# Optimization experiments

Hardware: AMD Instinct MI355X
Metric: run time of the kernel (lower is better)

The kernel has to match this reference:

```python
import jax, jax.numpy as jnp
import numpy as np

SEQ_LENGTH = 256
MID_O = 800
OUT_DIM = 128

def _lstm_cell(x, h, c, Wih, Whh, bih, bhh):
    # PyTorch gate order: i, f, g, o
    gates = x @ Wih.T + h @ Whh.T + bih + bhh
    i, f, g, o = jnp.split(gates, 4, axis=-1)
    c = jax.nn.sigmoid(f) * c + jax.nn.sigmoid(i) * jnp.tanh(g)
    h = jax.nn.sigmoid(o) * jnp.tanh(c)
    return h, c

def _lstm_layer(x_seq, Wih, Whh, bih, bhh):
    B = x_seq.shape[1]
    H = Whh.shape[1]
    h0 = jnp.zeros((B, H), x_seq.dtype)
    c0 = jnp.zeros((B, H), x_seq.dtype)
    def step(carry, xt):
        h, c = carry
        h, c = _lstm_cell(xt, h, c, Wih, Whh, bih, bhh)
        return (h, c), h
    (hT, cT), out = jax.lax.scan(step, (h0, c0), x_seq)
    return out, hT, cT

def _lstm_params(key, in_dim, hid, scale=0.05):
    k1, k2, k3, k4 = jax.random.split(key, 4)
    return (jax.random.normal(k1, (4 * hid, in_dim), jnp.float32) * scale,
            jax.random.normal(k2, (4 * hid, hid), jnp.float32) * scale,
            jax.random.normal(k3, (4 * hid,), jnp.float32) * scale,
            jax.random.normal(k4, (4 * hid,), jnp.float32) * scale)

def setup_inputs() -> dict:
    key = jax.random.key(0)
    ks = jax.random.split(key, 10)
    input_dim, mid_i, latent, mid_o, out_dim = 128, 60, 20, MID_O, OUT_DIM
    x = jax.random.normal(ks[0], (SEQ_LENGTH, 1024, input_dim), jnp.float32)
    fc1 = _lstm_params(ks[1], input_dim, mid_i)
    fc21 = _lstm_params(ks[2], mid_i, latent)
    l3 = _lstm_params(ks[3], latent, latent)
    l4 = _lstm_params(ks[4], latent, mid_o)
    l5 = _lstm_params(ks[5], mid_o, out_dim)
    id_W = jax.random.normal(ks[6], (latent, latent), jnp.float32) * 0.05
    id_b = jnp.zeros((latent,), jnp.float32)
    down_W = jax.random.normal(ks[7], (latent, out_dim), jnp.float32) * 0.05
    down_b = jnp.zeros((latent,), jnp.float32)
    d = {"x": x,
         "fc1_Wih": fc1[0], "fc1_Whh": fc1[1], "fc1_bih": fc1[2], "fc1_bhh": fc1[3],
         "fc21_Wih": fc21[0], "fc21_Whh": fc21[1], "fc21_bih": fc21[2], "fc21_bhh": fc21[3],
         "l3_Wih": l3[0], "l3_Whh": l3[1], "l3_bih": l3[2], "l3_bhh": l3[3],
         "l4_Wih": l4[0], "l4_Whh": l4[1], "l4_bih": l4[2], "l4_bhh": l4[3],
         "l5_Wih": l5[0], "l5_Whh": l5[1], "l5_bih": l5[2], "l5_bhh": l5[3],
         "id_W": id_W, "id_b": id_b, "down_W": down_W, "down_b": down_b}
    return d

def reference(x, fc1_Wih, fc1_Whh, fc1_bih, fc1_bhh,
              fc21_Wih, fc21_Whh, fc21_bih, fc21_bhh,
              l3_Wih, l3_Whh, l3_bih, l3_bhh,
              l4_Wih, l4_Whh, l4_bih, l4_bhh,
              l5_Wih, l5_Whh, l5_bih, l5_bhh,
              id_W, id_b, down_W, down_b):
    # ---- encode ----
    out1, _, _ = _lstm_layer(x, fc1_Wih, fc1_Whh, fc1_bih, fc1_bhh)
    h1 = jax.nn.relu(out1)
    _, mu, c_mean = _lstm_layer(h1, fc21_Wih, fc21_Whh, fc21_bih, fc21_bhh)
    # ---- decode (deterministic: z = mu, c_t = cell_mean) ----
    B = mu.shape[0]
    output0 = mu @ id_W.T + id_b
    h2 = jnp.zeros((B, MID_O), x.dtype); c2 = jnp.zeros((B, MID_O), x.dtype)
    h3 = jnp.zeros((B, OUT_DIM), x.dtype); c3 = jnp.zeros((B, OUT_DIM), x.dtype)
    def step(carry, _):
        h, c, h2, c2, h3, c3, out = carry
        h, c = _lstm_cell(out, h, c, l3_Wih, l3_Whh, l3_bih, l3_bhh)
        h2, c2 = _lstm_cell(h, h2, c2, l4_Wih, l4_Whh, l4_bih, l4_bhh)
        h3, c3 = _lstm_cell(h2, h3, c3, l5_Wih, l5_Whh, l5_bih, l5_bhh)
        out = h3 @ down_W.T + down_b
        return (h, c, h2, c2, h3, c3, out), h3
    _, outMean = jax.lax.scan(step, (mu, c_mean, h2, c2, h3, c3, output0), None, length=SEQ_LENGTH)
    return outMean, mu
```

## Files before the change

### kernel.cpp

```cpp
#include <hip/hip_runtime.h>
#include <stdint.h>

typedef __bf16 bf16x8 __attribute__((ext_vector_type(8)));
typedef float  f32x4  __attribute__((ext_vector_type(4)));

static __device__ __forceinline__ unsigned short f2bf(float f) {
  unsigned int u = __float_as_uint(f);
  u = u + 0x7fffu + ((u >> 16) & 1u);
  return (unsigned short)(u >> 16);
}
static __device__ __forceinline__ float bf2f(unsigned short h) {
  return __uint_as_float(((unsigned int)h) << 16);
}
static __device__ __forceinline__ float sigm(float x) {
  return 1.f / (1.f + __expf(-x));
}
static __device__ __forceinline__ float tanh_f(float x) {
  float ax = fabsf(x);
  float e = __expf(-2.f * ax);
  float t = (1.f - e) / (1.f + e);
  return copysignf(t, x);
}

__global__ void kPrep(const float* __restrict__ w4i, const float* __restrict__ w4h,
                      const float* __restrict__ b4i, const float* __restrict__ b4h,
                      const float* __restrict__ w5i, const float* __restrict__ w5h,
                      const float* __restrict__ b5i, const float* __restrict__ b5h,
                      const float* __restrict__ w1i, const float* __restrict__ w1h,
                      const float* __restrict__ b1i, const float* __restrict__ b1h,
                      const float* __restrict__ w2i, const float* __restrict__ w2h,
                      const float* __restrict__ b2i, const float* __restrict__ b2h,
                      const float* __restrict__ w3i, const float* __restrict__ w3h,
                      const float* __restrict__ b3i, const float* __restrict__ b3h,
                      unsigned short* __restrict__ W4F, unsigned short* __restrict__ W5,
                      float* __restrict__ W1, float* __restrict__ W2, float* __restrict__ W3,
                      float* __restrict__ b4, float* __restrict__ b5,
                      float* __restrict__ b1, float* __restrict__ b2, float* __restrict__ b3) {
  int idx0 = blockIdx.x * blockDim.x + threadIdx.x;
  int stride = gridDim.x * blockDim.x;
  const int TOT = 3197328;
  for (int i = idx0; i < TOT; i += stride) {
    int i2 = i;
    if (i2 < 2662400) {
      int T = i2 / 13312;
      int r1 = i2 % 13312;
      int kc = r1 / 512;
      int e = r1 % 512;
      int lane = e >> 3, j = e & 7;
      int q = lane >> 4, l16 = lane & 15;
      int gate = ((T & 1) ? 2 : 0) + (l16 >> 3);
      int col = (T >> 1) * 8 + (l16 & 7);
      int wrow = gate * 800 + col;
      int k = kc * 32 + q * 8 + j;
      float v = (k < 20) ? w4i[wrow * 20 + k]
                         : ((k >= 24 && k < 824) ? w4h[wrow * 800 + (k - 24)] : 0.f);
      W4F[i2] = f2bf(v);
      continue;
    }
    i2 -= 2662400;
    if (i2 < 475136) {
      int n = i2 / 928, k = i2 % 928;
      float v = (k < 800) ? w5i[n * 800 + k] : w5h[n * 128 + (k - 800)];
      W5[i2] = f2bf(v);
      continue;
    }
    i2 -= 475136;
    if (i2 < 46080) {
      int n = i2 / 192, k = i2 % 192;
      W1[i2] = (k < 128) ? w1i[n * 128 + k] : ((k < 188) ? w1h[n * 60 + (k - 128)] : 0.f);
      continue;
    }
    i2 -= 46080;
    if (i2 < 6400) {
      int n = i2 / 80, k = i2 % 80;
      W2[i2] = (k < 60) ? w2i[n * 60 + k] : w2h[n * 20 + (k - 60)];
      continue;
    }
    i2 -= 6400;
    if (i2 < 3200) {
      int n = i2 / 40, k = i2 % 40;
      W3[i2] = (k < 20) ? w3i[n * 20 + k] : w3h[n * 20 + (k - 20)];
      continue;
    }
    i2 -= 3200;
    if (i2 < 3200) { b4[i2] = b4i[i2] + b4h[i2]; continue; }
    i2 -= 3200;
    if (i2 < 512) { b5[i2] = b5i[i2] + b5h[i2]; continue; }
    i2 -= 512;
    if (i2 < 240) { b1[i2] = b1i[i2] + b1h[i2]; continue; }
    i2 -= 240;
    if (i2 < 80) { b2[i2] = b2i[i2] + b2h[i2]; continue; }
    i2 -= 80;
    b3[i2] = b3i[i2] + b3h[i2];
  }
}

__global__ void kZero(unsigned int* __restrict__ pk, unsigned int* __restrict__ bf) {
  int idx = blockIdx.x * blockDim.x + threadIdx.x;
  int stride = gridDim.x * blockDim.x;
  for (int i = idx; i < 974848; i += stride) pk[i] = 0u;
  if (idx < 128) bf[idx] = 0u;
}

__global__ __launch_bounds__(256, 2)
void kEnc(const float* __restrict__ x,
          const float* __restrict__ W1, const float* __restrict__ b1,
          const float* __restrict__ W2, const float* __restrict__ b2,
          const float* __restrict__ idW, const float* __restrict__ idb,
          float* __restrict__ hl30, float* __restrict__ cl30,
          float* __restrict__ out0, float* __restrict__ muOut) {
  __shared__ float xb[512];
  __shared__ float hb[240], cbb[240], h1b[240];
  __shared__ float h21[80], c21[80];
  __shared__ float g1[960], g2[320];
  const int tid = threadIdx.x;
  const int rowbase = blockIdx.x * 4;
  if (tid < 240) { hb[tid] = 0.f; cbb[tid] = 0.f; h1b[tid] = 0.f; }
  if (tid < 80) { h21[tid] = 0.f; c21[tid] = 0.f; }
  __syncthreads();
  for (int t = 0; t < 256; ++t) {
    const float* xs = x + ((size_t)t * 1024 + rowbase) * 128;
    xb[tid] = xs[tid];
    xb[tid + 256] = xs[tid + 256];
    __syncthreads();
    if (tid < 240) {
      const float* wr = W1 + tid * 192;
      float s0 = b1[tid], s1 = s0, s2 = s0, s3 = s0;
      for (int k = 0; k < 128; ++k) {
        float w = wr[k];
        s0 += w * xb[k]; s1 += w * xb[128 + k]; s2 += w * xb[256 + k]; s3 += w * xb[384 + k];
      }
      for (int k = 0; k < 60; ++k) {
        float w = wr[128 + k];
        s0 += w * hb[k]; s1 += w * hb[60 + k]; s2 += w * hb[120 + k]; s3 += w * hb[180 + k];
      }
      g1[tid] = s0; g1[240 + tid] = s1; g1[480 + tid] = s2; g1[720 + tid] = s3;
    }
    __syncthreads();
    if (tid < 240) {
      int b = tid / 60, j = tid % 60;
      const float* g = g1 + b * 240;
      float iv = sigm(g[j]), fv = sigm(g[60 + j]), gv = tanh_f(g[120 + j]), ov = sigm(g[180 + j]);
      float c = fv * cbb[b * 60 + j] + iv * gv;
      cbb[b * 60 + j] = c;
      float h = ov * tanh_f(c);
      hb[b * 60 + j] = h;
      h1b[b * 60 + j] = fmaxf(h, 0.f);
    }
    __syncthreads();
    if (tid < 80) {
      const float* wr = W2 + tid * 80;
      float s0 = b2[tid], s1 = s0, s2 = s0, s3 = s0;
      for (int k = 0; k < 60; ++k) {
        float w = wr[k];
        s0 += w * h1b[k]; s1 += w * h1b[60 + k]; s2 += w * h1b[120 + k]; s3 += w * h1b[180 + k];
      }
      for (int k = 0; k < 20; ++k) {
        float w = wr[60 + k];
        s0 += w * h21[k]; s1 += w * h21[20 + k]; s2 += w * h21[40 + k]; s3 += w * h21[60 + k];
      }
      g2[tid] = s0; g2[80 + tid] = s1; g2[160 + tid] = s2; g2[240 + tid] = s3;
    }
    __syncthreads();
    if (tid < 80) {
      int b = tid / 20, j = tid % 20;
      const float* g = g2 + b * 80;
      float iv = sigm(g[j]), fv = sigm(g[20 + j]), gv = tanh_f(g[40 + j]), ov = sigm(g[60 + j]);
      float c = fv * c21[b * 20 + j] + iv * gv;
      c21[b * 20 + j] = c;
      h21[b * 20 + j] = ov * tanh_f(c);
    }
    __syncthreads();
  }
  if (tid < 80) {
    int b = tid / 20, j = tid % 20;
    int gb = rowbase + b;
    float mu = h21[b * 20 + j];
    muOut[(size_t)gb * 20 + j] = mu;
    hl30[gb * 20 + j] = mu;
    cl30[gb * 20 + j] = c21[b * 20 + j];
    float s = idb[j];
    for (int k = 0; k < 20; ++k) s += h21[b * 20 + k] * idW[j * 20 + k];
    out0[gb * 20 + j] = s;
  }
}

#define NBLK 256

static __device__ __forceinline__ void gbar(unsigned int* bar, unsigned int target) {
  __syncthreads();
  if (threadIdx.x == 0) {
    __hip_atomic_fetch_add(bar, 1u, __ATOMIC_RELEASE, __HIP_MEMORY_SCOPE_AGENT);
    while (__hip_atomic_load(bar, __ATOMIC_RELAXED, __HIP_MEMORY_SCOPE_AGENT) < target)
      __builtin_amdgcn_s_sleep(1);
    (void)__hip_atomic_load(bar, __ATOMIC_ACQUIRE, __HIP_MEMORY_SCOPE_AGENT);
  }
  __syncthreads();
}

__global__ __launch_bounds__(256, 1)
void kDec(const unsigned short* __restrict__ W4F, const float* __restrict__ b4,
          const unsigned short* __restrict__ W5, const float* __restrict__ b5,
          const float* __restrict__ W3g, const float* __restrict__ b3g,
          const float* __restrict__ dWg, const float* __restrict__ dbg,
          const float* __restrict__ out0, const float* __restrict__ hl3g,
          const float* __restrict__ cl3g,
          unsigned short* __restrict__ pk0, unsigned short* __restrict__ pk1,
          float* __restrict__ dout, unsigned int* __restrict__ barflag) {
  __shared__ __align__(16) char smem[59792];
  unsigned int* bar = barflag;
  unsigned int* flag = barflag + 64;

  const int tid = threadIdx.x;
  const int b = blockIdx.x;
  const int lane = tid & 63, wv = tid >> 6;
  const int q = lane >> 4, l16 = lane & 15;

  float* red = (float*)(smem + 49552);
  float* S = (float*)smem;
  float* lsHl = S;
  float* lsCl = S + 640;
  float* lsOut = S + 1280;
  float* lsG = S + 1920;
  float* lsW3 = S + 4480;
  float* lsb3 = S + 7680;
  float* lsdW = S + 7760;
  float* lsdb = S + 10320;
  unsigned short* lsH3 = (unsigned short*)(S + 10340);

  const bool isL4 = (b < 200);
  const bool isL3 = (b >= 200) && (b < 232);

  const int cg = b % 25, rg = b / 25;
  const int colOct = cg * 4 + wv;
  const int col4 = colOct * 8 + (l16 & 7);
  const bool lo = (l16 & 8) == 0;
  bf16x8 B40[26], B41[26];
  float bb0 = 0.f, bb1 = 0.f;
  float c2reg[32];
  if (isL4) {
    const int T0 = cg * 8 + wv * 2;
    const unsigned short* p0 = W4F + (size_t)T0 * 13312 + lane * 8;
    const unsigned short* p1 = W4F + (size_t)(T0 + 1) * 13312 + lane * 8;
#pragma unroll
    for (int kc = 0; kc < 26; ++kc) {
      B40[kc] = *(const bf16x8*)(p0 + kc * 512);
      B41[kc] = *(const bf16x8*)(p1 + kc * 512);
    }
    const int g0 = (l16 >> 3), g1 = 2 + (l16 >> 3);
    bb0 = b4[g0 * 800 + col4];
    bb1 = b4[g1 * 800 + col4];
#pragma unroll
    for (int i = 0; i < 32; ++i) c2reg[i] = 0.f;
  }
  const int rb3 = (b - 200) * 32;
  if (isL3) {
    for (int i = tid; i < 3200; i += 256) lsW3[i] = W3g[i];
    for (int i = tid; i < 2560; i += 256) lsdW[i] = dWg[i];
    if (tid < 80) lsb3[tid] = b3g[tid];
    if (tid < 20) lsdb[tid] = dbg[tid];
    for (int i = tid; i < 640; i += 256) {
      lsHl[i] = hl3g[rb3 * 20 + i];
      lsCl[i] = cl3g[rb3 * 20 + i];
    }
  }
  const int ry = b >> 3, jx = b & 7;
  const int rowf = wv & 1, kh = wv >> 1;
  const int rb5 = ry * 32 + rowf * 16;
  const int u5 = jx * 16 + l16;
  float c3reg[4] = {0.f, 0.f, 0.f, 0.f};
  const float bi5 = b5[u5], bf5 = b5[128 + u5], bg5 = b5[256 + u5], bo5 = b5[384 + u5];
  const size_t Aoff5 = (size_t)(rb5 + l16) * 952 + 24 + q * 8;
  const unsigned short* Brow5[4];
#pragma unroll
  for (int g = 0; g < 4; ++g) Brow5[g] = W5 + (size_t)(g * 128 + u5) * 928 + q * 8;

  __syncthreads();

  unsigned int barTarget = 0;
  for (int t = 0; t < 256; ++t) {
    unsigned short* pkR = (t & 1) ? pk1 : pk0;
    unsigned short* pkW = (t & 1) ? pk0 : pk1;
    if (isL3) {
      if (t == 0) {
        for (int i = tid; i < 640; i += 256) lsOut[i] = out0[rb3 * 20 + i];
      } else {
        for (int i = tid; i < 512; i += 256) {
          int r = i >> 4, s = i & 15;
          *(uint4*)(lsH3 + r * 128 + s * 8) =
              *(const uint4*)(pkR + (size_t)(rb3 + r) * 952 + 824 + s * 8);
        }
        __syncthreads();
        for (int i = tid; i < 640; i += 256) {
          int r = i / 20, k = i - r * 20;
          const unsigned short* hr = lsH3 + r * 128;
          const float* wr = lsdW + k * 128;
          float s = lsdb[k];
          for (int j = 0; j < 128; ++j) s += bf2f(hr[j]) * wr[j];
          lsOut[i] = s;
        }
      }
      __syncthreads();
      for (int i = tid; i < 2560; i += 256) {
        int r = i / 80, n = i - r * 80;
        const float* wr = lsW3 + n * 40;
        const float* ob = lsOut + r * 20;
        const float* hp = lsHl + r * 20;
        float s = lsb3[n];
#pragma unroll
        for (int k = 0; k < 20; ++k) s += ob[k] * wr[k];
#pragma unroll
        for (int k = 0; k < 20; ++k) s += hp[k] * wr[20 + k];
        lsG[i] = s;
      }
      __syncthreads();
      for (int i = tid; i < 640; i += 256) {
        int r = i / 20, j = i - r * 20;
        const float* g = lsG + r * 80;
        float cv = sigm(g[20 + j]) * lsCl[i] + sigm(g[j]) * tanh_f(g[40 + j]);
        float hv = sigm(g[60 + j]) * tanh_f(cv);
        lsCl[i] = cv;
        lsHl[i] = hv;
        pkR[(size_t)(rb3 + r) * 952 + j] = f2bf(hv);
      }
      __syncthreads();
      if (tid == 0)
        __hip_atomic_fetch_add(flag, 1u, __ATOMIC_RELEASE, __HIP_MEMORY_SCOPE_AGENT);
    } else if (isL4) {
      f32x4 acc[8][2];
#pragma unroll
      for (int mi = 0; mi < 8; ++mi) {
        acc[mi][0] = (f32x4){0.f, 0.f, 0.f, 0.f};
        acc[mi][1] = (f32x4){0.f, 0.f, 0.f, 0.f};
      }
      const unsigned short* Ab = pkR + (size_t)(rg * 128 + l16) * 952 + q * 8;
#pragma unroll
      for (int kc = 1; kc < 26; ++kc) {
        bf16x8 a[8];
#pragma unroll
        for (int mi = 0; mi < 8; ++mi)
          a[mi] = *(const bf16x8*)(Ab + (size_t)mi * 15232 + kc * 32);
#pragma unroll
        for (int mi = 0; mi < 8; ++mi) {
          acc[mi][0] = __builtin_amdgcn_mfma_f32_16x16x32_bf16(a[mi], B40[kc], acc[mi][0], 0, 0, 0);
          acc[mi][1] = __builtin_amdgcn_mfma_f32_16x16x32_bf16(a[mi], B41[kc], acc[mi][1], 0, 0, 0);
        }
      }
      if (tid == 0) {
        while (__hip_atomic_load(flag, __ATOMIC_RELAXED, __HIP_MEMORY_SCOPE_AGENT) < 32u * (t + 1))
          __builtin_amdgcn_s_sleep(1);
        (void)__hip_atomic_load(flag, __ATOMIC_ACQUIRE, __HIP_MEMORY_SCOPE_AGENT);
      }
      __syncthreads();
#pragma unroll
      for (int mi = 0; mi < 8; ++mi) {
        bf16x8 a0 = *(const bf16x8*)(Ab + (size_t)mi * 15232);
        acc[mi][0] = __builtin_amdgcn_mfma_f32_16x16x32_bf16(a0, B40[0], acc[mi][0], 0, 0, 0);
        acc[mi][1] = __builtin_amdgcn_mfma_f32_16x16x32_bf16(a0, B41[0], acc[mi][1], 0, 0, 0);
      }
#pragma unroll
      for (int mi = 0; mi < 8; ++mi) {
#pragma unroll
        for (int r = 0; r < 4; ++r) {
          float v0 = acc[mi][0][r] + bb0;
          float v1 = acc[mi][1][r] + bb1;
          float p0 = __shfl_xor(v0, 8);
          float p1 = __shfl_xor(v1, 8);
          float iv = sigm(lo ? v0 : p0);
          float fv = sigm(lo ? p0 : v0);
          float gv = tanh_f(lo ? v1 : p1);
          float ov = sigm(lo ? p1 : v1);
          float cv = fv * c2reg[mi * 4 + r] + iv * gv;
          c2reg[mi * 4 + r] = cv;
          float hv = ov * tanh_f(cv);
          if (lo)
            pkW[(size_t)(rg * 128 + mi * 16 + q * 4 + r) * 952 + 24 + col4] = f2bf(hv);
        }
      }
    }
    barTarget += NBLK;
    gbar(bar, barTarget);
    {
      f32x4 a5[4];
#pragma unroll
      for (int g = 0; g < 4; ++g) a5[g] = (f32x4){0.f, 0.f, 0.f, 0.f};
      const int kcB = kh ? 15 : 0, kcE = kh ? 25 : 15;
      for (int kc = kcB; kc < kcE; ++kc) {
        bf16x8 av = *(const bf16x8*)(pkW + Aoff5 + kc * 32);
#pragma unroll
        for (int g = 0; g < 4; ++g) {
          bf16x8 bv = *(const bf16x8*)(Brow5[g] + kc * 32);
          a5[g] = __builtin_amdgcn_mfma_f32_16x16x32_bf16(av, bv, a5[g], 0, 0, 0);
        }
      }
      if (kh) {
        for (int kc = 25; kc < 29; ++kc) {
          bf16x8 av = *(const bf16x8*)(pkR + Aoff5 + kc * 32);
#pragma unroll
          for (int g = 0; g < 4; ++g) {
            bf16x8 bv = *(const bf16x8*)(Brow5[g] + kc * 32);
            a5[g] = __builtin_amdgcn_mfma_f32_16x16x32_bf16(av, bv, a5[g], 0, 0, 0);
          }
        }
        float* myred = red + (rowf * 64 + lane) * 20;
#pragma unroll
        for (int g = 0; g < 4; ++g) *(f32x4*)(myred + g * 4) = a5[g];
      }
      __syncthreads();
      if (!kh) {
        const float* myred = red + (rowf * 64 + lane) * 20;
#pragma unroll
        for (int g = 0; g < 4; ++g) a5[g] += *(const f32x4*)(myred + g * 4);
#pragma unroll
        for (int r = 0; r < 4; ++r) {
          int row = rb5 + q * 4 + r;
          float iv = sigm(a5[0][r] + bi5);
          float fv = sigm(a5[1][r] + bf5);
          float gv = tanh_f(a5[2][r] + bg5);
          float ov = sigm(a5[3][r] + bo5);
          float cv = fv * c3reg[r] + iv * gv;
          c3reg[r] = cv;
          float hv = ov * tanh_f(cv);
          dout[(size_t)t * 131072 + (size_t)row * 128 + u5] = hv;
          pkW[(size_t)row * 952 + 824 + u5] = f2bf(hv);
        }
      }
    }
    barTarget += NBLK;
    if (t < 255) gbar(bar, barTarget);
  }
}

extern "C" void kernel_launch(void* const* d_in, const int* in_sizes, int n_in,
                              void* d_out, int out_size, void* d_ws, size_t ws_size,
                              hipStream_t stream) {
  (void)in_sizes; (void)n_in; (void)out_size; (void)ws_size;
  const float* x   = (const float*)d_in[0];
  const float* w1i = (const float*)d_in[1];
  const float* w1h = (const float*)d_in[2];
  const float* b1i = (const float*)d_in[3];
  const float* b1h = (const float*)d_in[4];
  const float* w2i = (const float*)d_in[5];
  const float* w2h = (const float*)d_in[6];
  const float* b2i = (const float*)d_in[7];
  const float* b2h = (const float*)d_in[8];
  const float* w3i = (const float*)d_in[9];
  const float* w3h = (const float*)d_in[10];
  const float* b3i = (const float*)d_in[11];
  const float* b3h = (const float*)d_in[12];
  const float* w4i = (const float*)d_in[13];
  const float* w4h = (const float*)d_in[14];
  const float* b4i = (const float*)d_in[15];
  const float* b4h = (const float*)d_in[16];
  const float* w5i = (const float*)d_in[17];
  const float* w5h = (const float*)d_in[18];
  const float* b5i = (const float*)d_in[19];
  const float* b5h = (const float*)d_in[20];
  const float* idW = (const float*)d_in[21];
  const float* idb = (const float*)d_in[22];
  const float* dWp = (const float*)d_in[23];
  const float* dbp = (const float*)d_in[24];
  float* out = (float*)d_out;

  char* ws = (char*)d_ws;
  size_t off = 0;
  auto alloc = [&](size_t bytes) -> void* {
    void* p = ws + off;
    off = (off + bytes + 255) & ~(size_t)255;
    return p;
  };
  unsigned short* W4F = (unsigned short*)alloc(3200 * 832 * 2);
  unsigned short* W5 = (unsigned short*)alloc(512 * 928 * 2);
  float* W1 = (float*)alloc(240 * 192 * 4);
  float* W2 = (float*)alloc(80 * 80 * 4);
  float* W3 = (float*)alloc(80 * 40 * 4);
  float* b4 = (float*)alloc(3200 * 4);
  float* b5 = (float*)alloc(512 * 4);
  float* b1 = (float*)alloc(240 * 4);
  float* b2 = (float*)alloc(80 * 4);
  float* b3 = (float*)alloc(80 * 4);
  unsigned short* pk0 = (unsigned short*)alloc((size_t)1024 * 952 * 2);
  unsigned short* pk1 = (unsigned short*)alloc((size_t)1024 * 952 * 2);
  float* hl3 = (float*)alloc(1024 * 20 * 4);
  float* cl3 = (float*)alloc(1024 * 20 * 4);
  float* out0 = (float*)alloc(1024 * 20 * 4);
  unsigned int* barflag = (unsigned int*)alloc(512);

  kPrep<<<dim3(4096), dim3(256), 0, stream>>>(
      w4i, w4h, b4i, b4h, w5i, w5h, b5i, b5h, w1i, w1h, b1i, b1h,
      w2i, w2h, b2i, b2h, w3i, w3h, b3i, b3h,
      W4F, W5, W1, W2, W3, b4, b5, b1, b2, b3);
  kZero<<<dim3(1024), dim3(256), 0, stream>>>((unsigned int*)pk0, barflag);
  kEnc<<<dim3(256), dim3(256), 0, stream>>>(x, W1, b1, W2, b2, idW, idb,
                                            hl3, cl3, out0, out + 33554432);
  kDec<<<dim3(256), dim3(256), 0, stream>>>(W4F, b4, W5, b5, W3, b3, dWp, dbp,
                                            out0, hl3, cl3, pk0, pk1, out, barflag);
}
```

Before: 24.76 ms.

## Double decoder block to 8 waves, one weight tile per wave for layer 4

The persistent decoder kernel now launches 512 threads per block, not 256. Each wave holds a single register-resident layer-4 weight tile covering all four gates of 4 columns, instead of two tiles covering 8 columns. The prep kernel repacks W4 so each 16-lane group interleaves the i/f/g/o gates, and the gate values are gathered with three xor-shuffles. The aim is to halve per-wave register pressure and MFMA chain length and raise occupancy and latency hiding. The cost is idle extra waves in the layer-5 phase and more shuffles per element.

```diff
diff --git a/kernel.cpp b/kernel.cpp
--- a/kernel.cpp
+++ b/kernel.cpp
@@ -48,8 +48,8 @@
       int e = r1 % 512;
       int lane = e >> 3, j = e & 7;
       int q = lane >> 4, l16 = lane & 15;
-      int gate = ((T & 1) ? 2 : 0) + (l16 >> 3);
-      int col = (T >> 1) * 8 + (l16 & 7);
+      int gate = l16 >> 2;
+      int col = T * 4 + (l16 & 3);
       int wrow = gate * 800 + col;
       int k = kc * 32 + q * 8 + j;
       float v = (k < 20) ? w4i[wrow * 20 + k]
@@ -198,7 +198,7 @@
   __syncthreads();
 }
 
-__global__ __launch_bounds__(256, 1)
+__global__ __launch_bounds__(512, 2)
 void kDec(const unsigned short* __restrict__ W4F, const float* __restrict__ b4,
           const unsigned short* __restrict__ W5, const float* __restrict__ b5,
           const float* __restrict__ W3g, const float* __restrict__ b3g,
@@ -232,40 +232,34 @@
   const bool isL3 = (b >= 200) && (b < 232);
 
   const int cg = b % 25, rg = b / 25;
-  const int colOct = cg * 4 + wv;
-  const int col4 = colOct * 8 + (l16 & 7);
-  const bool lo = (l16 & 8) == 0;
-  bf16x8 B40[26], B41[26];
-  float bb0 = 0.f, bb1 = 0.f;
+  const int tc = cg * 8 + wv;
+  const int col4 = tc * 4 + (l16 & 3);
+  const bool gb0 = ((l16 >> 2) & 1) != 0;
+  const bool gb1 = ((l16 >> 3) & 1) != 0;
+  bf16x8 B4[26];
+  float bb = 0.f;
   float c2reg[32];
   if (isL4) {
-    const int T0 = cg * 8 + wv * 2;
-    const unsigned short* p0 = W4F + (size_t)T0 * 13312 + lane * 8;
-    const unsigned short* p1 = W4F + (size_t)(T0 + 1) * 13312 + lane * 8;
-#pragma unroll
-    for (int kc = 0; kc < 26; ++kc) {
-      B40[kc] = *(const bf16x8*)(p0 + kc * 512);
-      B41[kc] = *(const bf16x8*)(p1 + kc * 512);
-    }
-    const int g0 = (l16 >> 3), g1 = 2 + (l16 >> 3);
-    bb0 = b4[g0 * 800 + col4];
-    bb1 = b4[g1 * 800 + col4];
+    const unsigned short* p0 = W4F + (size_t)tc * 13312 + lane * 8;
+#pragma unroll
+    for (int kc = 0; kc < 26; ++kc) B4[kc] = *(const bf16x8*)(p0 + kc * 512);
+    bb = b4[(l16 >> 2) * 800 + col4];
 #pragma unroll
     for (int i = 0; i < 32; ++i) c2reg[i] = 0.f;
   }
   const int rb3 = (b - 200) * 32;
   if (isL3) {
-    for (int i = tid; i < 3200; i += 256) lsW3[i] = W3g[i];
-    for (int i = tid; i < 2560; i += 256) lsdW[i] = dWg[i];
+    for (int i = tid; i < 3200; i += 512) lsW3[i] = W3g[i];
+    for (int i = tid; i < 2560; i += 512) lsdW[i] = dWg[i];
     if (tid < 80) lsb3[tid] = b3g[tid];
     if (tid < 20) lsdb[tid] = dbg[tid];
-    for (int i = tid; i < 640; i += 256) {
+    for (int i = tid; i < 640; i += 512) {
       lsHl[i] = hl3g[rb3 * 20 + i];
       lsCl[i] = cl3g[rb3 * 20 + i];
     }
   }
   const int ry = b >> 3, jx = b & 7;
-  const int rowf = wv & 1, kh = wv >> 1;
+  const int rowf = wv & 1, kh = (wv >> 1) & 1;
   const int rb5 = ry * 32 + rowf * 16;
   const int u5 = jx * 16 + l16;
   float c3reg[4] = {0.f, 0.f, 0.f, 0.f};
@@ -283,15 +277,15 @@
     unsigned short* pkW = (t & 1) ? pk0 : pk1;
     if (isL3) {
       if (t == 0) {
-        for (int i = tid; i < 640; i += 256) lsOut[i] = out0[rb3 * 20 + i];
+        for (int i = tid; i < 640; i += 512) lsOut[i] = out0[rb3 * 20 + i];
       } else {
-        for (int i = tid; i < 512; i += 256) {
+        for (int i = tid; i < 512; i += 512) {
           int r = i >> 4, s = i & 15;
           *(uint4*)(lsH3 + r * 128 + s * 8) =
               *(const uint4*)(pkR + (size_t)(rb3 + r) * 952 + 824 + s * 8);
         }
         __syncthreads();
-        for (int i = tid; i < 640; i += 256) {
+        for (int i = tid; i < 640; i += 512) {
           int r = i / 20, k = i - r * 20;
           const unsigned short* hr = lsH3 + r * 128;
           const float* wr = lsdW + k * 128;
@@ -301,7 +295,7 @@
         }
       }
       __syncthreads();
-      for (int i = tid; i < 2560; i += 256) {
+      for (int i = tid; i < 2560; i += 512) {
         int r = i / 80, n = i - r * 80;
         const float* wr = lsW3 + n * 40;
         const float* ob = lsOut + r * 20;
@@ -314,7 +308,7 @@
         lsG[i] = s;
       }
       __syncthreads();
-      for (int i = tid; i < 640; i += 256) {
+      for (int i = tid; i < 640; i += 512) {
         int r = i / 20, j = i - r * 20;
         const float* g = lsG + r * 80;
         float cv = sigm(g[20 + j]) * lsCl[i] + sigm(g[j]) * tanh_f(g[40 + j]);
@@ -327,23 +321,16 @@
       if (tid == 0)
         __hip_atomic_fetch_add(flag, 1u, __ATOMIC_RELEASE, __HIP_MEMORY_SCOPE_AGENT);
     } else if (isL4) {
-      f32x4 acc[8][2];
-#pragma unroll
-      for (int mi = 0; mi < 8; ++mi) {
-        acc[mi][0] = (f32x4){0.f, 0.f, 0.f, 0.f};
-        acc[mi][1] = (f32x4){0.f, 0.f, 0.f, 0.f};
-      }
+      f32x4 acc[8];
+#pragma unroll
+      for (int mi = 0; mi < 8; ++mi) acc[mi] = (f32x4){0.f, 0.f, 0.f, 0.f};
       const unsigned short* Ab = pkR + (size_t)(rg * 128 + l16) * 952 + q * 8;
 #pragma unroll
       for (int kc = 1; kc < 26; ++kc) {
-        bf16x8 a[8];
-#pragma unroll
-        for (int mi = 0; mi < 8; ++mi)
-          a[mi] = *(const bf16x8*)(Ab + (size_t)mi * 15232 + kc * 32);
 #pragma unroll
         for (int mi = 0; mi < 8; ++mi) {
-          acc[mi][0] = __builtin_amdgcn_mfma_f32_16x16x32_bf16(a[mi], B40[kc], acc[mi][0], 0, 0, 0);
-          acc[mi][1] = __builtin_amdgcn_mfma_f32_16x16x32_bf16(a[mi], B41[kc], acc[mi][1], 0, 0, 0);
+          bf16x8 a = *(const bf16x8*)(Ab + (size_t)mi * 15232 + kc * 32);
+          acc[mi] = __builtin_amdgcn_mfma_f32_16x16x32_bf16(a, B4[kc], acc[mi], 0, 0, 0);
         }
       }
       if (tid == 0) {
@@ -355,25 +342,25 @@
 #pragma unroll
       for (int mi = 0; mi < 8; ++mi) {
         bf16x8 a0 = *(const bf16x8*)(Ab + (size_t)mi * 15232);
-        acc[mi][0] = __builtin_amdgcn_mfma_f32_16x16x32_bf16(a0, B40[0], acc[mi][0], 0, 0, 0);
-        acc[mi][1] = __builtin_amdgcn_mfma_f32_16x16x32_bf16(a0, B41[0], acc[mi][1], 0, 0, 0);
+        acc[mi] = __builtin_amdgcn_mfma_f32_16x16x32_bf16(a0, B4[0], acc[mi], 0, 0, 0);
       }
 #pragma unroll
       for (int mi = 0; mi < 8; ++mi) {
 #pragma unroll
         for (int r = 0; r < 4; ++r) {
-          float v0 = acc[mi][0][r] + bb0;
-          float v1 = acc[mi][1][r] + bb1;
-          float p0 = __shfl_xor(v0, 8);
-          float p1 = __shfl_xor(v1, 8);
-          float iv = sigm(lo ? v0 : p0);
-          float fv = sigm(lo ? p0 : v0);
-          float gv = tanh_f(lo ? v1 : p1);
-          float ov = sigm(lo ? p1 : v1);
+          float v = acc[mi][r] + bb;
+          float x1 = __shfl_xor(v, 4);
+          float x2 = __shfl_xor(v, 8);
+          float x3 = __shfl_xor(x1, 8);
+          float iv = gb1 ? (gb0 ? x3 : x2) : (gb0 ? x1 : v);
+          float fv = gb1 ? (gb0 ? x2 : x3) : (gb0 ? v : x1);
+          float gv = gb1 ? (gb0 ? x1 : v) : (gb0 ? x3 : x2);
+          float ov = gb1 ? (gb0 ? v : x1) : (gb0 ? x2 : x3);
+          iv = sigm(iv); fv = sigm(fv); gv = tanh_f(gv); ov = sigm(ov);
           float cv = fv * c2reg[mi * 4 + r] + iv * gv;
           c2reg[mi * 4 + r] = cv;
           float hv = ov * tanh_f(cv);
-          if (lo)
+          if (l16 < 4)
             pkW[(size_t)(rg * 128 + mi * 16 + q * 4 + r) * 952 + 24 + col4] = f2bf(hv);
         }
       }
@@ -381,49 +368,53 @@
     barTarget += NBLK;
     gbar(bar, barTarget);
     {
-      f32x4 a5[4];
-#pragma unroll
-      for (int g = 0; g < 4; ++g) a5[g] = (f32x4){0.f, 0.f, 0.f, 0.f};
-      const int kcB = kh ? 15 : 0, kcE = kh ? 25 : 15;
-      for (int kc = kcB; kc < kcE; ++kc) {
-        bf16x8 av = *(const bf16x8*)(pkW + Aoff5 + kc * 32);
-#pragma unroll
-        for (int g = 0; g < 4; ++g) {
-          bf16x8 bv = *(const bf16x8*)(Brow5[g] + kc * 32);
-          a5[g] = __builtin_amdgcn_mfma_f32_16x16x32_bf16(av, bv, a5[g], 0, 0, 0);
-        }
-      }
-      if (kh) {
-        for (int kc = 25; kc < 29; ++kc) {
-          bf16x8 av = *(const bf16x8*)(pkR + Aoff5 + kc * 32);
+      if (wv < 4) {
+        f32x4 a5[4];
+#pragma unroll
+        for (int g = 0; g < 4; ++g) a5[g] = (f32x4){0.f, 0.f, 0.f, 0.f};
+        const int kcB = kh ? 15 : 0, kcE = kh ? 25 : 15;
+        for (int kc = kcB; kc < kcE; ++kc) {
+          bf16x8 av = *(const bf16x8*)(pkW + Aoff5 + kc * 32);
 #pragma unroll
           for (int g = 0; g < 4; ++g) {
             bf16x8 bv = *(const bf16x8*)(Brow5[g] + kc * 32);
             a5[g] = __builtin_amdgcn_mfma_f32_16x16x32_bf16(av, bv, a5[g], 0, 0, 0);
           }
         }
-        float* myred = red + (rowf * 64 + lane) * 20;
-#pragma unroll
-        for (int g = 0; g < 4; ++g) *(f32x4*)(myred + g * 4) = a5[g];
-      }
-      __syncthreads();
-      if (!kh) {
-        const float* myred = red + (rowf * 64 + lane) * 20;
-#pragma unroll
-        for (int g = 0; g < 4; ++g) a5[g] += *(const f32x4*)(myred + g * 4);
-#pragma unroll
-        for (int r = 0; r < 4; ++r) {
-          int row = rb5 + q * 4 + r;
-          float iv = sigm(a5[0][r] + bi5);
-          float fv = sigm(a5[1][r] + bf5);
-          float gv = tanh_f(a5[2][r] + bg5);
-          float ov = sigm(a5[3][r] + bo5);
-          float cv = fv * c3reg[r] + iv * gv;
-          c3reg[r] = cv;
-          float hv = ov * tanh_f(cv);
-          dout[(size_t)t * 131072 + (size_t)row * 128 + u5] = hv;
-          pkW[(size_t)row * 952 + 824 + u5] = f2bf(hv);
-        }
+        if (kh) {
+          for (int kc = 25; kc < 29; ++kc) {
+            bf16x8 av = *(const bf16x8*)(pkR + Aoff5 + kc * 32);
+#pragma unroll
+            for (int g = 0; g < 4; ++g) {
+              bf16x8 bv = *(const bf16x8*)(Brow5[g] + kc * 32);
+              a5[g] = __builtin_amdgcn_mfma_f32_16x16x32_bf16(av, bv, a5[g], 0, 0, 0);
+            }
+          }
+          float* myred = red + (rowf * 64 + lane) * 20;
+#pragma unroll
+          for (int g = 0; g < 4; ++g) *(f32x4*)(myred + g * 4) = a5[g];
+        }
+        __syncthreads();
+        if (!kh) {
+          const float* myred = red + (rowf * 64 + lane) * 20;
+#pragma unroll
+          for (int g = 0; g < 4; ++g) a5[g] += *(const f32x4*)(myred + g * 4);
+#pragma unroll
+          for (int r = 0; r < 4; ++r) {
+            int row = rb5 + q * 4 + r;
+            float iv = sigm(a5[0][r] + bi5);
+            float fv = sigm(a5[1][r] + bf5);
+            float gv = tanh_f(a5[2][r] + bg5);
+            float ov = sigm(a5[3][r] + bo5);
+            float cv = fv * c3reg[r] + iv * gv;
+            c3reg[r] = cv;
+            float hv = ov * tanh_f(cv);
+            dout[(size_t)t * 131072 + (size_t)row * 128 + u5] = hv;
+            pkW[(size_t)row * 952 + 824 + u5] = f2bf(hv);
+          }
+        }
+      } else {
+        __syncthreads();
       }
     }
     barTarget += NBLK;
@@ -493,6 +484,6 @@
   kZero<<<dim3(1024), dim3(256), 0, stream>>>((unsigned int*)pk0, barflag);
   kEnc<<<dim3(256), dim3(256), 0, stream>>>(x, W1, b1, W2, b2, idW, idb,
                                             hl3, cl3, out0, out + 33554432);
-  kDec<<<dim3(256), dim3(256), 0, stream>>>(W4F, b4, W5, b5, W3, b3, dWp, dbp,
+  kDec<<<dim3(256), dim3(512), 0, stream>>>(W4F, b4, W5, b5, W3, b3, dWp, dbp,
                                             out0, hl3, cl3, pk0, pk1, out, barflag);
 }
```

Result: slower. 27.46 ms (+10.9%).
